# Optimization experiments

Hardware: AMD Instinct MI355X
Metric: run time of the kernel (lower is better)

## Reference

```python
import jax, jax.numpy as jnp
import numpy as np

B, N, C = 8, 16384, 64
NUM_HEADS = 1
SR = 8
HEAD_DIM = C // NUM_HEADS
SCALE = HEAD_DIM ** -0.5


def setup_inputs() -> dict:
    key = jax.random.key(0)
    ks = jax.random.split(key, 8)
    s = 0.02
    return {
        "x": jax.random.normal(ks[0], (B, N, C), dtype=jnp.float32),
        "H": 128,
        "W": 128,
        "w_q": jax.random.normal(ks[1], (C, C), dtype=jnp.float32) * s,
        "w_kv": jax.random.normal(ks[2], (2 * C, C), dtype=jnp.float32) * s,
        "w_sr": jax.random.normal(ks[3], (C, C, SR, SR), dtype=jnp.float32) * np.sqrt(2.0 / (SR * SR * C)).astype(np.float32),
        "b_sr": jnp.zeros((C,), dtype=jnp.float32),
        "ln_g": jnp.ones((C,), dtype=jnp.float32),
        "ln_b": jnp.zeros((C,), dtype=jnp.float32),
        "w_proj": jax.random.normal(ks[4], (C, C), dtype=jnp.float32) * s,
        "b_proj": jnp.zeros((C,), dtype=jnp.float32),
    }


def _layernorm(x, g, b, eps=1e-5):
    mu = jnp.mean(x, axis=-1, keepdims=True)
    var = jnp.var(x, axis=-1, keepdims=True)
    return (x - mu) * jax.lax.rsqrt(var + eps) * g + b


def reference(x, H, W, w_q, w_kv, w_sr, b_sr, ln_g, ln_b, w_proj, b_proj):
    Bsz, Ntok, Cdim = x.shape
    # q: [B, h, N, d]
    q = (x @ w_q.T).reshape(Bsz, Ntok, NUM_HEADS, HEAD_DIM).transpose(0, 2, 1, 3)
    # spatial reduction on kv: [B,N,C] -> [B,C,H,W] -> conv(k=s=SR) -> [B,N',C]
    kv_sp = x.transpose(0, 2, 1).reshape(Bsz, Cdim, H, W)
    kv_sp = jax.lax.conv_general_dilated(
        kv_sp, w_sr, window_strides=(SR, SR), padding="VALID",
        dimension_numbers=("NCHW", "OIHW", "NCHW"))
    kv_sp = kv_sp + b_sr[None, :, None, None]
    Np = kv_sp.shape[2] * kv_sp.shape[3]
    kv_tok = kv_sp.reshape(Bsz, Cdim, Np).transpose(0, 2, 1)  # [B, N', C]
    kv_tok = _layernorm(kv_tok, ln_g, ln_b)
    # kv projection -> k, v: [B, h, N', d]
    kv = (kv_tok @ w_kv.T).reshape(Bsz, Np, 2, NUM_HEADS, HEAD_DIM).transpose(2, 0, 3, 1, 4)
    k, v = kv[0], kv[1]
    # attention: [B, h, N, N']
    attn = jnp.einsum("bhnd,bhmd->bhnm", q * SCALE, k)
    attn = jax.nn.softmax(attn, axis=-1)
    out = jnp.einsum("bhnm,bhmd->bhnd", attn, v)
    out = out.transpose(0, 2, 1, 3).reshape(Bsz, Ntok, Cdim)
    return out @ w_proj.T + b_proj
```

## Files before the change

kernel.cpp:

```cpp
#include <hip/hip_runtime.h>
#include <hip/hip_bf16.h>

#define BATCH 8
#define NTOK 16384

typedef __attribute__((ext_vector_type(8))) short bf16x8;
typedef __attribute__((ext_vector_type(4))) short bf16x4;
typedef __attribute__((ext_vector_type(4))) float f32x4;
typedef __attribute__((ext_vector_type(4))) unsigned int u32x4;

#define MFMA(a, b, c) __builtin_amdgcn_mfma_f32_16x16x32_bf16(a, b, c, 0, 0, 0)

__device__ __forceinline__ short f2bf(float f) {
  unsigned u = __builtin_bit_cast(unsigned, f);
  u = (u + 0x7fffu + ((u >> 16) & 1u)) >> 16;
  return (short)u;
}
__device__ __forceinline__ bf16x8 cvt8(f32x4 v0, f32x4 v1) {
  bf16x8 a;
  a[0] = f2bf(v0[0]); a[1] = f2bf(v0[1]); a[2] = f2bf(v0[2]); a[3] = f2bf(v0[3]);
  a[4] = f2bf(v1[0]); a[5] = f2bf(v1[1]); a[6] = f2bf(v1[2]); a[7] = f2bf(v1[3]);
  return a;
}
__device__ __forceinline__ unsigned pk2(float a, float b) {
  __hip_bfloat162 h = __float22bfloat162_rn(float2{a, b});
  unsigned r;
  __builtin_memcpy(&r, &h, 4);
  return r;
}
__device__ __forceinline__ bf16x8 cvt8pk(f32x4 v0, f32x4 v1) {
  u32x4 w;
  w[0] = pk2(v0[0], v0[1]);
  w[1] = pk2(v0[2], v0[3]);
  w[2] = pk2(v1[1 - 1], v1[1]);
  w[3] = pk2(v1[2], v1[3]);
  return __builtin_bit_cast(bf16x8, w);
}

__global__ __launch_bounds__(256) void prep_k(const float* __restrict__ w_sr,
                                              short* __restrict__ W2T) {
  __shared__ float tile[64 * 65];
  const int o = blockIdx.x;
  const float* src = w_sr + (o << 12);
  short* dst = W2T + (o << 12);
  const int tid = threadIdx.x;
#pragma unroll
  for (int k = 0; k < 16; ++k) {
    int idx = k * 256 + tid;
    int c = idx >> 6, t = idx & 63;
    tile[c * 65 + t] = src[idx];
  }
  __syncthreads();
#pragma unroll
  for (int k = 0; k < 16; ++k) {
    int idx = k * 256 + tid;
    int t = idx >> 6, c = idx & 63;
    dst[idx] = f2bf(tile[c * 65 + t]);
  }
}

__global__ __launch_bounds__(256, 4) void conv_k(const float* __restrict__ x,
                                                 const short* __restrict__ W2T,
                                                 float* __restrict__ convP) {
  __shared__ short Axl[2 * 128 * 64];
  const int tid = threadIdx.x;
  const int lane = tid & 63;
  const int nt = tid >> 6;
  const int g = lane >> 4;
  const int kq = lane & 15;
  const int pblk = blockIdx.x >> 2;
  const int split = blockIdx.x & 3;
  const int pbase = pblk << 4;
  const int b = pbase >> 8;
  const int pi = pblk & 15;
  const size_t xb = (size_t)b * NTOK * 64;
  const int y0 = pi * 8 + split * 2;

#pragma unroll
  for (int i = 0; i < 8; ++i) {
    int cid = i * 256 + tid;
    int row = cid >> 3;
    int ti = row >> 7, col = row & 127;
    int slot = (cid & 7) ^ ((col >> 3) & 7);
    const float* src = x + xb + ((size_t)((y0 + ti) * 128 + col) << 6) + ((cid & 7) << 3);
    bf16x8 v = cvt8(*(const f32x4*)src, *(const f32x4*)(src + 4));
    *(bf16x8*)(&Axl[(row << 6) + (slot << 3)]) = v;
  }
  __syncthreads();

  f32x4 acc = (f32x4){0.f, 0.f, 0.f, 0.f};
  const int c0 = split << 5;
#pragma unroll 4
  for (int c32 = c0; c32 < c0 + 32; ++c32) {
    int t = c32 >> 1;
    int ti = (t >> 3) & 1;
    int tj = t & 7;
    int row = ti * 128 + kq * 8 + tj;
    int slot = (((c32 & 1) << 2) + g) ^ (kq & 7);
    bf16x8 a = *(const bf16x8*)(&Axl[(row << 6) + (slot << 3)]);
    bf16x8 wb = *(const bf16x8*)(W2T + ((nt * 16 + kq) << 12) + (c32 << 5) + (g << 3));
    acc = MFMA(a, wb, acc);
  }
#pragma unroll
  for (int r = 0; r < 4; ++r) {
    int prow = pbase + g * 4 + r;
    convP[((split << 11) + prow) * 64 + nt * 16 + kq] = acc[r];
  }
}

__global__ __launch_bounds__(256) void kvkq_k(
    const float* __restrict__ convP, const float* __restrict__ b_sr,
    const float* __restrict__ ln_g, const float* __restrict__ ln_b,
    const float* __restrict__ w_kv, const float* __restrict__ w_q,
    const float* __restrict__ w_proj, short* __restrict__ KQ,
    short* __restrict__ VPT) {
  __shared__ float wT[64 * 128];
  __shared__ float wq[64 * 64];
  __shared__ float wp[64 * 64];
  __shared__ float rowz[8][64];
  __shared__ float Kf[8][68];
  __shared__ float Vf[8][68];
  const int tid = threadIdx.x;
#pragma unroll 8
  for (int i = 0; i < 32; ++i) {
    int idx = i * 256 + tid;
    int d2 = idx >> 6, c = idx & 63;
    wT[(c << 7) + (d2 ^ (c & 31))] = w_kv[idx];
  }
#pragma unroll
  for (int i = 0; i < 16; ++i) {
    int idx = i * 256 + tid;
    wq[idx] = w_q[idx] * 0.125f;
    wp[idx] = w_proj[idx];
  }
  const int gr0 = blockIdx.x << 3;
  const int b = gr0 >> 8;
  const int key0 = gr0 & 255;
  {
    const int c = tid & 63;
    const int w = tid >> 6;
#pragma unroll
    for (int pass = 0; pass < 2; ++pass) {
      int row = pass * 4 + w;
      int gr = gr0 + row;
      float y = b_sr[c];
#pragma unroll
      for (int s = 0; s < 4; ++s) y += convP[((s << 11) + gr) * 64 + c];
      float s1 = y, s2 = y * y;
#pragma unroll
      for (int off = 1; off < 64; off <<= 1) {
        s1 += __shfl_xor(s1, off);
        s2 += __shfl_xor(s2, off);
      }
      float mu = s1 * 0.015625f;
      float var = s2 * 0.015625f - mu * mu;
      float rs = rsqrtf(var + 1e-5f);
      rowz[row][c] = (y - mu) * rs * ln_g[c] + ln_b[c];
    }
  }
  __syncthreads();
  {
    const int row = tid >> 5;
    const int c4 = (tid & 31) * 4;
    float acc[4] = {0.f, 0.f, 0.f, 0.f};
#pragma unroll
    for (int c = 0; c < 64; ++c) {
      float rz = rowz[row][c];
#pragma unroll
      for (int j = 0; j < 4; ++j) acc[j] += rz * wT[(c << 7) + ((c4 + j) ^ (c & 31))];
    }
    if (c4 < 64) {
#pragma unroll
      for (int j = 0; j < 4; ++j) Kf[row][c4 + j] = acc[j];
    } else {
#pragma unroll
      for (int j = 0; j < 4; ++j) Vf[row][c4 - 64 + j] = acc[j];
    }
  }
  __syncthreads();
  {
    const int row = tid >> 5;
    const int cc2 = (tid & 31) * 2;
    float a[2] = {0.f, 0.f};
#pragma unroll
    for (int o = 0; o < 64; ++o) {
      float kv = Kf[row][o];
#pragma unroll
      for (int j = 0; j < 2; ++j) a[j] += kv * wq[o * 64 + cc2 + j];
    }
    short* dst = KQ + (size_t)(gr0 + row) * 64 + cc2;
#pragma unroll
    for (int j = 0; j < 2; ++j) dst[j] = f2bf(a[j]);
  }
  {
    const int o = tid >> 2;
    const int k2 = (tid & 3) * 2;
    float v[2] = {0.f, 0.f};
#pragma unroll
    for (int d = 0; d < 64; ++d) {
      float wv = wp[o * 64 + d];
#pragma unroll
      for (int j = 0; j < 2; ++j) v[j] += wv * Vf[k2 + j][d];
    }
    short* dst = VPT + ((size_t)b << 14) + o * 256 + key0 + k2;
#pragma unroll
    for (int j = 0; j < 2; ++j) dst[j] = f2bf(v[j]);
  }
}

__global__ __launch_bounds__(512, 2) void attn_k(
    const float* __restrict__ x, const short* __restrict__ KQ,
    const short* __restrict__ VPT, const float* __restrict__ bproj,
    float* __restrict__ out) {
  __shared__ short KQl[256 * 64];
  __shared__ short VPTl[64 * 264];

  const int tid = threadIdx.x;
  const int lane = tid & 63;
  const int wid = tid >> 6;
  const int b = blockIdx.x >> 6;
  const int n0 = (blockIdx.x & 63) << 8;
  const int g = lane >> 4;
  const int kq = lane & 15;
  const int tok0 = n0 + wid * 32;
  const size_t xbase = ((size_t)b * NTOK + tok0) * 64;

  bf16x8 xa[2][2];
#pragma unroll
  for (int m = 0; m < 2; ++m)
#pragma unroll
    for (int kc = 0; kc < 2; ++kc) {
      const float* p = x + xbase + (size_t)(m * 16 + kq) * 64 + kc * 32 + g * 8;
      xa[m][kc] = cvt8pk(*(const f32x4*)p, *(const f32x4*)(p + 4));
    }
  float bp[4];
#pragma unroll
  for (int nd = 0; nd < 4; ++nd) bp[nd] = bproj[nd * 16 + kq];

  {
    const uint4* Kg = (const uint4*)(KQ + ((size_t)b << 14));
#pragma unroll
    for (int i = 0; i < 4; ++i) {
      int id = i * 512 + tid;
      int row = id >> 3, s = id & 7;
      *(uint4*)(&KQl[(row << 6) + ((s ^ (row & 7)) << 3)]) = Kg[id];
    }
    const uint4* Vg = (const uint4*)(VPT + ((size_t)b << 14));
#pragma unroll
    for (int i = 0; i < 4; ++i) {
      int id = i * 512 + tid;
      int o = id >> 5, s = id & 31;
      uint4 v = Vg[id];
      int p0 = (2 * s) ^ (o & 7);
      int p1 = (2 * s + 1) ^ (o & 7);
      uint2 lo; lo.x = v.x; lo.y = v.y;
      uint2 hi; hi.x = v.z; hi.y = v.w;
      *(uint2*)(&VPTl[o * 264 + p0 * 4]) = lo;
      *(uint2*)(&VPTl[o * 264 + p1 * 4]) = hi;
    }
  }
  __syncthreads();

  f32x4 pv[2][4];
  f32x4 pvs[2];
#pragma unroll
  for (int m = 0; m < 2; ++m) {
#pragma unroll
    for (int nd = 0; nd < 4; ++nd) pv[m][nd] = (f32x4){0.f, 0.f, 0.f, 0.f};
    pvs[m] = (f32x4){0.f, 0.f, 0.f, 0.f};
  }
  const short one_bf = (short)0x3F80;
  const bf16x8 ones8 = (bf16x8){one_bf, one_bf, one_bf, one_bf,
                                one_bf, one_bf, one_bf, one_bf};

  auto qkchunk = [&](int C, f32x4 (&S)[2][2]) {
#pragma unroll
    for (int kk = 0; kk < 2; ++kk) {
      int key = (2 * C + kk) * 16 + kq;
      bf16x8 kb0 = *(const bf16x8*)(&KQl[(key << 6) + (((0 + g) ^ (key & 7)) << 3)]);
      bf16x8 kb1 = *(const bf16x8*)(&KQl[(key << 6) + (((4 + g) ^ (key & 7)) << 3)]);
#pragma unroll
      for (int m = 0; m < 2; ++m) {
        f32x4 s4 = MFMA(kb0, xa[m][0], ((f32x4){0.f, 0.f, 0.f, 0.f}));
        S[m][kk] = MFMA(kb1, xa[m][1], s4);
      }
    }
  };

  f32x4 scur[2][2], snxt[2][2];
  qkchunk(0, scur);

  __builtin_amdgcn_s_setprio(1);
#pragma unroll
  for (int c = 0; c < 8; ++c) {
    if (c < 7) qkchunk(c + 1, snxt);
    bf16x8 a8[2];
#pragma unroll
    for (int m = 0; m < 2; ++m) {
      f32x4 e0, e1;
#pragma unroll
      for (int r = 0; r < 4; ++r) e0[r] = __expf(scur[m][0][r]);
#pragma unroll
      for (int r = 0; r < 4; ++r) e1[r] = __expf(scur[m][1][r]);
      u32x4 w;
      w[0] = pk2(e0[0], e0[1]);
      w[1] = pk2(e0[2], e0[3]);
      w[2] = pk2(e1[0], e1[1]);
      w[3] = pk2(e1[2], e1[3]);
      a8[m] = __builtin_bit_cast(bf16x8, w);
    }
#pragma unroll
    for (int nd = 0; nd < 4; ++nd) {
      int o = nd * 16 + kq;
      const short* vrow = &VPTl[o * 264];
      int pa = (8 * c + g) ^ (o & 7);
      int pb_ = (8 * c + g + 4) ^ (o & 7);
      bf16x4 lo = *(const bf16x4*)(vrow + pa * 4);
      bf16x4 hi = *(const bf16x4*)(vrow + pb_ * 4);
      bf16x8 vb = (bf16x8){lo[0], lo[1], lo[2], lo[3], hi[0], hi[1], hi[2], hi[3]};
#pragma unroll
      for (int m = 0; m < 2; ++m) pv[m][nd] = MFMA(a8[m], vb, pv[m][nd]);
    }
#pragma unroll
    for (int m = 0; m < 2; ++m) pvs[m] = MFMA(a8[m], ones8, pvs[m]);
#pragma unroll
    for (int m = 0; m < 2; ++m) {
      scur[m][0] = snxt[m][0];
      scur[m][1] = snxt[m][1];
    }
  }
  __builtin_amdgcn_s_setprio(0);

#pragma unroll
  for (int m = 0; m < 2; ++m)
#pragma unroll
    for (int r = 0; r < 4; ++r) {
      float iv = 1.0f / pvs[m][r];
      size_t rowoff = xbase + (size_t)(m * 16 + g * 4 + r) * 64;
#pragma unroll
      for (int nd = 0; nd < 4; ++nd)
        out[rowoff + nd * 16 + kq] = pv[m][nd][r] * iv + bp[nd];
    }
}

extern "C" void kernel_launch(void* const* d_in, const int* in_sizes, int n_in,
                              void* d_out, int out_size, void* d_ws, size_t ws_size,
                              hipStream_t stream) {
  const float* x = (const float*)d_in[0];
  const float* w_q = (const float*)d_in[3];
  const float* w_kv = (const float*)d_in[4];
  const float* w_sr = (const float*)d_in[5];
  const float* b_sr = (const float*)d_in[6];
  const float* ln_g = (const float*)d_in[7];
  const float* ln_b = (const float*)d_in[8];
  const float* w_proj = (const float*)d_in[9];
  const float* b_proj = (const float*)d_in[10];
  float* out = (float*)d_out;

  char* ws = (char*)d_ws;
  short* W2T = (short*)(ws);
  short* KQ = (short*)(ws);
  short* VPT = (short*)(ws + 262144);
  float* convP = (float*)(ws + 524288);

  hipLaunchKernelGGL(prep_k, dim3(64), dim3(256), 0, stream, w_sr, W2T);
  hipLaunchKernelGGL(conv_k, dim3(512), dim3(256), 0, stream, x, W2T, convP);
  hipLaunchKernelGGL(kvkq_k, dim3(256), dim3(256), 0, stream, convP, b_sr, ln_g,
                     ln_b, w_kv, w_q, w_proj, KQ, VPT);
  hipLaunchKernelGGL(attn_k, dim3(512), dim3(512), 0, stream, x, KQ, VPT,
                     b_proj, out);
}
```

Before: 45.67 us.

## Split attention work across 16 waves with 16 tokens each, dropping QK prefetch

```diff
diff --git a/kernel.cpp b/kernel.cpp
--- a/kernel.cpp
+++ b/kernel.cpp
@@ -32,7 +32,7 @@
   u32x4 w;
   w[0] = pk2(v0[0], v0[1]);
   w[1] = pk2(v0[2], v0[3]);
-  w[2] = pk2(v1[1 - 1], v1[1]);
+  w[2] = pk2(v1[0], v1[1]);
   w[3] = pk2(v1[2], v1[3]);
   return __builtin_bit_cast(bf16x8, w);
 }
@@ -208,7 +208,7 @@
   }
 }
 
-__global__ __launch_bounds__(512, 2) void attn_k(
+__global__ __launch_bounds__(1024, 2) void attn_k(
     const float* __restrict__ x, const short* __restrict__ KQ,
     const short* __restrict__ VPT, const float* __restrict__ bproj,
     float* __restrict__ out) {
@@ -222,17 +222,15 @@
   const int n0 = (blockIdx.x & 63) << 8;
   const int g = lane >> 4;
   const int kq = lane & 15;
-  const int tok0 = n0 + wid * 32;
+  const int tok0 = n0 + wid * 16;
   const size_t xbase = ((size_t)b * NTOK + tok0) * 64;
 
-  bf16x8 xa[2][2];
-#pragma unroll
-  for (int m = 0; m < 2; ++m)
-#pragma unroll
-    for (int kc = 0; kc < 2; ++kc) {
-      const float* p = x + xbase + (size_t)(m * 16 + kq) * 64 + kc * 32 + g * 8;
-      xa[m][kc] = cvt8pk(*(const f32x4*)p, *(const f32x4*)(p + 4));
-    }
+  bf16x8 xa[2];
+#pragma unroll
+  for (int kc = 0; kc < 2; ++kc) {
+    const float* p = x + xbase + (size_t)kq * 64 + kc * 32 + g * 8;
+    xa[kc] = cvt8pk(*(const f32x4*)p, *(const f32x4*)(p + 4));
+  }
   float bp[4];
 #pragma unroll
   for (int nd = 0; nd < 4; ++nd) bp[nd] = bproj[nd * 16 + kq];
@@ -240,15 +238,15 @@
   {
     const uint4* Kg = (const uint4*)(KQ + ((size_t)b << 14));
 #pragma unroll
-    for (int i = 0; i < 4; ++i) {
-      int id = i * 512 + tid;
+    for (int i = 0; i < 2; ++i) {
+      int id = i * 1024 + tid;
       int row = id >> 3, s = id & 7;
       *(uint4*)(&KQl[(row << 6) + ((s ^ (row & 7)) << 3)]) = Kg[id];
     }
     const uint4* Vg = (const uint4*)(VPT + ((size_t)b << 14));
 #pragma unroll
-    for (int i = 0; i < 4; ++i) {
-      int id = i * 512 + tid;
+    for (int i = 0; i < 2; ++i) {
+      int id = i * 1024 + tid;
       int o = id >> 5, s = id & 31;
       uint4 v = Vg[id];
       int p0 = (2 * s) ^ (o & 7);
@@ -261,86 +259,58 @@
   }
   __syncthreads();
 
-  f32x4 pv[2][4];
-  f32x4 pvs[2];
-#pragma unroll
-  for (int m = 0; m < 2; ++m) {
-#pragma unroll
-    for (int nd = 0; nd < 4; ++nd) pv[m][nd] = (f32x4){0.f, 0.f, 0.f, 0.f};
-    pvs[m] = (f32x4){0.f, 0.f, 0.f, 0.f};
-  }
+  f32x4 pv[4];
+  f32x4 pvs;
+#pragma unroll
+  for (int nd = 0; nd < 4; ++nd) pv[nd] = (f32x4){0.f, 0.f, 0.f, 0.f};
+  pvs = (f32x4){0.f, 0.f, 0.f, 0.f};
   const short one_bf = (short)0x3F80;
   const bf16x8 ones8 = (bf16x8){one_bf, one_bf, one_bf, one_bf,
                                 one_bf, one_bf, one_bf, one_bf};
 
-  auto qkchunk = [&](int C, f32x4 (&S)[2][2]) {
-#pragma unroll
-    for (int kk = 0; kk < 2; ++kk) {
-      int key = (2 * C + kk) * 16 + kq;
-      bf16x8 kb0 = *(const bf16x8*)(&KQl[(key << 6) + (((0 + g) ^ (key & 7)) << 3)]);
-      bf16x8 kb1 = *(const bf16x8*)(&KQl[(key << 6) + (((4 + g) ^ (key & 7)) << 3)]);
-#pragma unroll
-      for (int m = 0; m < 2; ++m) {
-        f32x4 s4 = MFMA(kb0, xa[m][0], ((f32x4){0.f, 0.f, 0.f, 0.f}));
-        S[m][kk] = MFMA(kb1, xa[m][1], s4);
+  f32x4 epair[2];
+#pragma unroll
+  for (int kt = 0; kt < 16; ++kt) {
+    int key = kt * 16 + kq;
+    bf16x8 kb0 = *(const bf16x8*)(&KQl[(key << 6) + (((0 + g) ^ (key & 7)) << 3)]);
+    bf16x8 kb1 = *(const bf16x8*)(&KQl[(key << 6) + (((4 + g) ^ (key & 7)) << 3)]);
+    f32x4 s4 = MFMA(kb0, xa[0], ((f32x4){0.f, 0.f, 0.f, 0.f}));
+    s4 = MFMA(kb1, xa[1], s4);
+    f32x4 e4;
+#pragma unroll
+    for (int r = 0; r < 4; ++r) e4[r] = __expf(s4[r]);
+    epair[kt & 1] = e4;
+    if (kt & 1) {
+      int c = kt >> 1;
+      u32x4 w;
+      w[0] = pk2(epair[0][0], epair[0][1]);
+      w[1] = pk2(epair[0][2], epair[0][3]);
+      w[2] = pk2(epair[1][0], epair[1][1]);
+      w[3] = pk2(epair[1][2], epair[1][3]);
+      bf16x8 a8 = __builtin_bit_cast(bf16x8, w);
+#pragma unroll
+      for (int nd = 0; nd < 4; ++nd) {
+        int o = nd * 16 + kq;
+        const short* vrow = &VPTl[o * 264];
+        int pa = (8 * c + g) ^ (o & 7);
+        int pb_ = (8 * c + g + 4) ^ (o & 7);
+        bf16x4 lo = *(const bf16x4*)(vrow + pa * 4);
+        bf16x4 hi = *(const bf16x4*)(vrow + pb_ * 4);
+        bf16x8 vb = (bf16x8){lo[0], lo[1], lo[2], lo[3], hi[0], hi[1], hi[2], hi[3]};
+        pv[nd] = MFMA(a8, vb, pv[nd]);
       }
-    }
-  };
-
-  f32x4 scur[2][2], snxt[2][2];
-  qkchunk(0, scur);
-
-  __builtin_amdgcn_s_setprio(1);
-#pragma unroll
-  for (int c = 0; c < 8; ++c) {
-    if (c < 7) qkchunk(c + 1, snxt);
-    bf16x8 a8[2];
-#pragma unroll
-    for (int m = 0; m < 2; ++m) {
-      f32x4 e0, e1;
-#pragma unroll
-      for (int r = 0; r < 4; ++r) e0[r] = __expf(scur[m][0][r]);
-#pragma unroll
-      for (int r = 0; r < 4; ++r) e1[r] = __expf(scur[m][1][r]);
-      u32x4 w;
-      w[0] = pk2(e0[0], e0[1]);
-      w[1] = pk2(e0[2], e0[3]);
-      w[2] = pk2(e1[0], e1[1]);
-      w[3] = pk2(e1[2], e1[3]);
-      a8[m] = __builtin_bit_cast(bf16x8, w);
-    }
-#pragma unroll
-    for (int nd = 0; nd < 4; ++nd) {
-      int o = nd * 16 + kq;
-      const short* vrow = &VPTl[o * 264];
-      int pa = (8 * c + g) ^ (o & 7);
-      int pb_ = (8 * c + g + 4) ^ (o & 7);
-      bf16x4 lo = *(const bf16x4*)(vrow + pa * 4);
-      bf16x4 hi = *(const bf16x4*)(vrow + pb_ * 4);
-      bf16x8 vb = (bf16x8){lo[0], lo[1], lo[2], lo[3], hi[0], hi[1], hi[2], hi[3]};
-#pragma unroll
-      for (int m = 0; m < 2; ++m) pv[m][nd] = MFMA(a8[m], vb, pv[m][nd]);
-    }
-#pragma unroll
-    for (int m = 0; m < 2; ++m) pvs[m] = MFMA(a8[m], ones8, pvs[m]);
-#pragma unroll
-    for (int m = 0; m < 2; ++m) {
-      scur[m][0] = snxt[m][0];
-      scur[m][1] = snxt[m][1];
-    }
-  }
-  __builtin_amdgcn_s_setprio(0);
-
-#pragma unroll
-  for (int m = 0; m < 2; ++m)
-#pragma unroll
-    for (int r = 0; r < 4; ++r) {
-      float iv = 1.0f / pvs[m][r];
-      size_t rowoff = xbase + (size_t)(m * 16 + g * 4 + r) * 64;
-#pragma unroll
-      for (int nd = 0; nd < 4; ++nd)
-        out[rowoff + nd * 16 + kq] = pv[m][nd][r] * iv + bp[nd];
-    }
+      pvs = MFMA(a8, ones8, pvs);
+    }
+  }
+
+#pragma unroll
+  for (int r = 0; r < 4; ++r) {
+    float iv = 1.0f / pvs[r];
+    size_t rowoff = xbase + (size_t)(g * 4 + r) * 64;
+#pragma unroll
+    for (int nd = 0; nd < 4; ++nd)
+      out[rowoff + nd * 16 + kq] = pv[nd][r] * iv + bp[nd];
+  }
 }
 
 extern "C" void kernel_launch(void* const* d_in, const int* in_sizes, int n_in,
@@ -367,6 +337,6 @@
   hipLaunchKernelGGL(conv_k, dim3(512), dim3(256), 0, stream, x, W2T, convP);
   hipLaunchKernelGGL(kvkq_k, dim3(256), dim3(256), 0, stream, convP, b_sr, ln_g,
                      ln_b, w_kv, w_q, w_proj, KQ, VPT);
-  hipLaunchKernelGGL(attn_k, dim3(512), dim3(512), 0, stream, x, KQ, VPT,
+  hipLaunchKernelGGL(attn_k, dim3(512), dim3(1024), 0, stream, x, KQ, VPT,
                      b_proj, out);
 }
```

Measured after the change: 48.31 us. 5.8% more time.
